# Kernel tuning notes

Measured on AMD Instinct MI355X. Metric: run time of the kernel, lower is better.

## Reference

```python
import jax, jax.numpy as jnp
import numpy as np

B, C_IN, C_HID, H, W = 4, 512, 512, 64, 64


def setup_inputs() -> dict:
    key = jax.random.key(0)
    ks = jax.random.split(key, 9)
    s_in = 1.0 / np.sqrt(C_IN)
    s_hid = 1.0 / np.sqrt(C_HID)
    return {
        "inp": jax.random.normal(ks[0], (B, C_IN, H, W), dtype=jnp.float32),
        "Wk": jax.random.normal(ks[1], (C_HID, C_IN), dtype=jnp.float32) * s_in,
        "bk": jax.random.normal(ks[2], (C_HID,), dtype=jnp.float32) * 0.01,
        "Wq": jax.random.normal(ks[3], (C_HID, C_IN), dtype=jnp.float32) * s_in,
        "bq": jax.random.normal(ks[4], (C_HID,), dtype=jnp.float32) * 0.01,
        "Wv": jax.random.normal(ks[5], (C_HID, C_IN), dtype=jnp.float32) * s_in,
        "bv": jax.random.normal(ks[6], (C_HID,), dtype=jnp.float32) * 0.01,
        "Wo": jax.random.normal(ks[7], (C_IN, C_HID), dtype=jnp.float32) * s_hid,
        "bo": jax.random.normal(ks[8], (C_IN,), dtype=jnp.float32) * 0.01,
    }


def reference(inp, Wk, bk, Wq, bq, Wv, bv, Wo, bo):
    b, _, h, w = inp.shape
    n = h * w

    def conv1x1(x, Wt, bias):  # 1x1 conv == per-pixel GEMM
        return jnp.einsum('bchw,oc->bohw', x, Wt) + bias[None, :, None, None]

    k = conv1x1(inp, Wk, bk).reshape(b, C_HID, n)   # [B,Ch,N]
    q = conv1x1(inp, Wq, bq).reshape(b, C_HID, n)
    v = conv1x1(inp, Wv, bv).reshape(b, C_HID, n)

    scale = 1.0 / jnp.sqrt(jnp.asarray(C_HID, dtype=jnp.float32))
    # weight[b,i,j] = <key_i, query_j> / sqrt(Ch); softmax over j (dim=2)
    scores = jnp.einsum('bci,bcj->bij', k, q) * scale  # [B,N,N]
    weight = jax.nn.softmax(scores, axis=2)
    # out[b,c,i] = sum_j weight[b,i,j] * v[b,c,j]
    out = jnp.einsum('bij,bcj->bci', weight, v).reshape(b, C_HID, h, w)
    return conv1x1(out, Wo, bo)  # [B,C_in,H,W]
```

## Files before the change

kernel.cpp:

```cpp
#include <hip/hip_runtime.h>
#include <hip/hip_bf16.h>


typedef __attribute__((ext_vector_type(4))) float f32x4;
typedef __attribute__((ext_vector_type(8))) short short8;
typedef __attribute__((ext_vector_type(4))) short short4v;

#define QSCALE 0.06376639774f

__device__ __forceinline__ unsigned short f2bf(float f) {
  unsigned u = __builtin_bit_cast(unsigned, f);
  unsigned r = (u + 0x7FFFu + ((u >> 16) & 1u)) >> 16;
  return (unsigned short)r;
}

__device__ __forceinline__ void gll16(const void* g, void* l) {
  __builtin_amdgcn_global_load_lds((const __attribute__((address_space(1))) void*)g,
                                   (__attribute__((address_space(3))) void*)l, 16, 0, 0);
}

__device__ __forceinline__ void gemm_core(const short* __restrict__ A, int lda,
                                          const short* __restrict__ B, int ldb,
                                          int nk, short* lds, f32x4 (&acc)[4][4]) {
  const int tid = threadIdx.x, w = tid >> 6, lane = tid & 63;
  const int g = lane >> 4, l15 = lane & 15;
  const int wr = w >> 1, wc = w & 1;
  const int rsub = lane >> 2, slot = lane & 3;
  char* la = (char*)lds;
  char* lb = (char*)(lds + 128 * 32);
  for (int ki = 0; ki < nk; ++ki) {
    const int k0 = ki * 32;
    __syncthreads();
#pragma unroll
    for (int q = 0; q < 2; ++q) {
      int qq = w * 2 + q;
      int row = qq * 16 + rsub;
      int soff = ((slot ^ (row & 3)) * 16);
      gll16((const char*)(A + (size_t)row * lda + k0) + soff, la + qq * 1024);
      gll16((const char*)(B + (size_t)row * ldb + k0) + soff, lb + qq * 1024);
    }
    __syncthreads();
    short8 am[4], bn[4];
#pragma unroll
    for (int m = 0; m < 4; ++m) {
      int row = wr * 64 + m * 16 + l15;
      am[m] = *(const short8*)(la + row * 64 + ((g * 16) ^ ((l15 & 3) << 4)));
    }
#pragma unroll
    for (int n = 0; n < 4; ++n) {
      int row = wc * 64 + n * 16 + l15;
      bn[n] = *(const short8*)(lb + row * 64 + ((g * 16) ^ ((l15 & 3) << 4)));
    }
#pragma unroll
    for (int m = 0; m < 4; ++m)
#pragma unroll
      for (int n = 0; n < 4; ++n)
        acc[m][n] = __builtin_amdgcn_mfma_f32_16x16x32_bf16(am[m], bn[n], acc[m][n], 0, 0, 0);
  }
}

#define BOUNCE_WRITE(lds2, row, col, val) \
  (lds2)[(row) * 128 + ((col) ^ (((row) & 7) << 3))] = (val)

#define BOUNCE_FLUSH(lds2, gbase, pitch)                                        \
  do {                                                                          \
    __syncthreads();                                                            \
    _Pragma("unroll")                                                           \
    for (int it_ = 0; it_ < 8; ++it_) {                                         \
      int row_ = (threadIdx.x >> 4) + it_ * 16;                                 \
      short8 v_ = *(const short8*)&(lds2)[row_ * 128 +                          \
                      (((threadIdx.x & 15) * 8) ^ ((row_ & 7) << 3))];          \
      *(short8*)((gbase) + (size_t)row_ * (pitch) + (threadIdx.x & 15) * 8) = v_;\
    }                                                                           \
  } while (0)

__global__ __launch_bounds__(256) void cvt_w_kernel(
    const float* __restrict__ wk, const float* __restrict__ wq,
    const float* __restrict__ wv, const float* __restrict__ wo,
    short* __restrict__ o) {
  int z = blockIdx.y;
  const float* s = (z == 0) ? wk : (z == 1) ? wq : (z == 2) ? wv : wo;
  int i = blockIdx.x * 256 + threadIdx.x;
  float4 f = ((const float4*)s)[i];
  short4v v;
  v[0] = (short)f2bf(f.x); v[1] = (short)f2bf(f.y);
  v[2] = (short)f2bf(f.z); v[3] = (short)f2bf(f.w);
  if (z < 3) {
    *(short4v*)(o + z * 262144 + i * 4) = v;
  } else {
    int idx = i * 4, co = idx >> 9, cc = idx & 511;
    short* base = o + 786432 + co * 1024 + cc;
    *(short4v*)base = v;
    *(short4v*)(base + 512) = v;
  }
}

__global__ __launch_bounds__(256) void transpose_x_kernel(
    const float* __restrict__ inp, short* __restrict__ xt) {
  __shared__ float t[32][33];
  int tx = threadIdx.x, ty = threadIdx.y;
  int n0 = blockIdx.x * 32, c0 = blockIdx.y * 32, b = blockIdx.z;
  const float* src = inp + ((size_t)(b * 512 + c0)) * 4096 + n0;
#pragma unroll
  for (int r = 0; r < 4; ++r) t[ty + r * 8][tx] = src[(ty + r * 8) * 4096 + tx];
  __syncthreads();
  short* dst = xt + ((size_t)((b << 12) + n0)) * 512 + c0;
#pragma unroll
  for (int r = 0; r < 4; ++r) dst[(ty + r * 8) * 512 + tx] = (short)f2bf(t[tx][ty + r * 8]);
}

__global__ __launch_bounds__(256) void gemm_kqv_kernel(
    const short* __restrict__ xt,
    const short* __restrict__ wk, const short* __restrict__ wq, const short* __restrict__ wv,
    const float* __restrict__ bk, const float* __restrict__ bq, const float* __restrict__ bv,
    short* __restrict__ kt, short* __restrict__ qt, short* __restrict__ vc) {
  const int z = blockIdx.z;
  __shared__ short lds[2 * 128 * 32];
  __shared__ short lds2[128 * 128];
  const short *A, *B;
  int arow0, brow0;
  if (z < 2) { arow0 = blockIdx.x * 128; brow0 = blockIdx.y * 128;
               A = xt + (size_t)arow0 * 512; B = ((z == 0) ? wk : wq) + (size_t)brow0 * 512; }
  else       { arow0 = blockIdx.y * 128; brow0 = blockIdx.x * 128;
               A = wv + (size_t)arow0 * 512; B = xt + (size_t)brow0 * 512; }
  f32x4 acc[4][4] = {};
  gemm_core(A, 512, B, 512, 16, lds, acc);
  const int tid = threadIdx.x, w = tid >> 6, lane = tid & 63;
  const int g = lane >> 4, l15 = lane & 15;
  const int wr = w >> 1, wc = w & 1;
#pragma unroll
  for (int m = 0; m < 4; ++m)
#pragma unroll
    for (int n = 0; n < 4; ++n)
#pragma unroll
      for (int r = 0; r < 4; ++r) {
        int row = wr * 64 + m * 16 + g * 4 + r, col = wc * 64 + n * 16 + l15;
        float v = acc[m][n][r], val;
        if (z == 0)      val = (v + bk[brow0 + col]) * QSCALE;
        else if (z == 1) val = v + bq[brow0 + col];
        else             val = v + bv[arow0 + row];
        BOUNCE_WRITE(lds2, row, col, (short)f2bf(val));
      }
  short* gbase; int pitch;
  if (z == 0)      { gbase = kt + (size_t)arow0 * 512 + brow0; pitch = 512; }
  else if (z == 1) { gbase = qt + (size_t)arow0 * 512 + brow0; pitch = 512; }
  else             { gbase = vc + (size_t)arow0 * 16384 + brow0; pitch = 16384; }
  BOUNCE_FLUSH(lds2, gbase, pitch);
}

__global__ __launch_bounds__(256) void gemm_s_kernel(
    const short* __restrict__ kt, const short* __restrict__ qt,
    short* __restrict__ P, float* __restrict__ Lpart) {
  __shared__ short lds[2 * 128 * 32];
  __shared__ short lds2[128 * 128];
  const int b = blockIdx.z & 3, h = blockIdx.z >> 2;
  const int i0 = blockIdx.y * 128, jl0 = blockIdx.x * 128;
  const int jg0 = h * 2048 + jl0;
  const short* A = kt + ((size_t)(b << 12) + i0) * 512;
  const short* B = qt + ((size_t)(b << 12) + jg0) * 512;
  f32x4 acc[4][4] = {};
  gemm_core(A, 512, B, 512, 16, lds, acc);
  const int tid = threadIdx.x, w = tid >> 6, lane = tid & 63;
  const int g = lane >> 4, l15 = lane & 15;
  const int wr = w >> 1, wc = w & 1;
  float rs[4][4];
#pragma unroll
  for (int m = 0; m < 4; ++m)
#pragma unroll
    for (int r = 0; r < 4; ++r) rs[m][r] = 0.f;
#pragma unroll
  for (int m = 0; m < 4; ++m)
#pragma unroll
    for (int n = 0; n < 4; ++n)
#pragma unroll
      for (int r = 0; r < 4; ++r) {
        float p = exp2f(acc[m][n][r]);
        rs[m][r] += p;
        int row = wr * 64 + m * 16 + g * 4 + r, col = wc * 64 + n * 16 + l15;
        BOUNCE_WRITE(lds2, row, col, (short)f2bf(p));
      }
  const int jp = (jg0 >> 6) + wc;
  float* Lp = Lpart + (((size_t)b * 64 + jp) << 12) + i0 + wr * 64;
#pragma unroll
  for (int m = 0; m < 4; ++m)
#pragma unroll
    for (int r = 0; r < 4; ++r) {
      float s = rs[m][r];
      s += __shfl_xor(s, 1); s += __shfl_xor(s, 2);
      s += __shfl_xor(s, 4); s += __shfl_xor(s, 8);
      if (l15 == 0) Lp[m * 16 + g * 4 + r] = s;
    }
  short* gbase = P + (size_t)h * 33554432 + ((size_t)((b << 12) + i0)) * 2048 + jl0;
  BOUNCE_FLUSH(lds2, gbase, 2048);
}

__global__ __launch_bounds__(256) void gemm_pv_kernel(
    const short* __restrict__ P, const short* __restrict__ vc,
    short* __restrict__ otab) {
  __shared__ short lds[2 * 128 * 32];
  __shared__ short lds2[128 * 128];
  const int bid = blockIdx.x;
  const int xcd = bid & 7, s = bid >> 3;
  const int c = s & 3, gi = (s >> 2) * 8 + xcd;
  const int i = gi & 31, bh = gi >> 5;
  const int b = bh & 3, h = bh >> 2;
  const int i0 = i * 128, c0 = c * 128;
  const short* A = P + (size_t)h * 33554432 + ((size_t)((b << 12) + i0)) * 2048;
  const short* B = vc + (size_t)c0 * 16384 + (b << 12) + h * 2048;
  f32x4 acc[4][4] = {};
  gemm_core(A, 2048, B, 16384, 64, lds, acc);
  const int tid = threadIdx.x, w = tid >> 6, lane = tid & 63;
  const int g = lane >> 4, l15 = lane & 15;
  const int wr = w >> 1, wc = w & 1;
#pragma unroll
  for (int m = 0; m < 4; ++m)
#pragma unroll
    for (int n = 0; n < 4; ++n)
#pragma unroll
      for (int r = 0; r < 4; ++r) {
        int row = wr * 64 + m * 16 + g * 4 + r, col = wc * 64 + n * 16 + l15;
        BOUNCE_WRITE(lds2, row, col, (short)f2bf(acc[m][n][r]));
      }
  short* gbase = otab + ((size_t)((b << 12) + i0)) * 1024 + h * 512 + c0;
  BOUNCE_FLUSH(lds2, gbase, 1024);
}

__global__ __launch_bounds__(256) void lred_kernel(
    const float* __restrict__ Lpart, float* __restrict__ linv) {
  int i = blockIdx.x * 256 + threadIdx.x;
  int b = i >> 12;
  float s = 0.f;
#pragma unroll 8
  for (int jp = 0; jp < 64; ++jp) s += Lpart[(((size_t)b * 64 + jp) << 12) + (i & 4095)];
  linv[i] = 1.0f / s;
}

__global__ __launch_bounds__(256) void gemm_out_kernel(
    const short* __restrict__ wdup, const short* __restrict__ otab,
    const float* __restrict__ bo, const float* __restrict__ linv,
    float* __restrict__ out) {
  __shared__ short lds[2 * 128 * 32];
  const int b = blockIdx.z;
  const int arow0 = blockIdx.y * 128;
  const int bn0 = blockIdx.x * 128;
  const short* A = wdup + (size_t)arow0 * 1024;
  const short* B = otab + ((size_t)((b << 12) + bn0)) * 1024;
  f32x4 acc[4][4] = {};
  gemm_core(A, 1024, B, 1024, 32, lds, acc);
  const int tid = threadIdx.x, w = tid >> 6, lane = tid & 63;
  const int g = lane >> 4, l15 = lane & 15;
  const int wr = w >> 1, wc = w & 1;
#pragma unroll
  for (int m = 0; m < 4; ++m) {
    int co = arow0 + wr * 64 + m * 16 + g * 4;
#pragma unroll
    for (int n = 0; n < 4; ++n) {
      int nl = bn0 + wc * 64 + n * 16 + l15;
      float li = linv[(b << 12) + nl];
#pragma unroll
      for (int r = 0; r < 4; ++r)
        out[((size_t)(b * 512 + co + r) << 12) + nl] = acc[m][n][r] * li + bo[co + r];
    }
  }
}

extern "C" void kernel_launch(void* const* d_in, const int* in_sizes, int n_in,
                              void* d_out, int out_size, void* d_ws, size_t ws_size,
                              hipStream_t stream) {
  const float* inp = (const float*)d_in[0];
  const float* Wk = (const float*)d_in[1];
  const float* bk = (const float*)d_in[2];
  const float* Wq = (const float*)d_in[3];
  const float* bq = (const float*)d_in[4];
  const float* Wv = (const float*)d_in[5];
  const float* bv = (const float*)d_in[6];
  const float* Wo = (const float*)d_in[7];
  const float* bo = (const float*)d_in[8];
  float* out = (float*)d_out;
  char* ws = (char*)d_ws;
  const size_t MB = 1048576;
  short* kt    = (short*)(ws);
  short* qt    = (short*)(ws + 16 * MB);
  short* vc    = (short*)(ws + 32 * MB);
  short* wb    = (short*)(ws + 48 * MB);
  short* xt    = (short*)(ws + 51 * MB);
  float* Lpart = (float*)(ws + 51 * MB);
  float* linv  = (float*)(ws + 55 * MB);
  short* P     = (short*)(ws + 67 * MB);
  short* otab  = (short*)(ws + 195 * MB);

  (void)in_sizes; (void)n_in; (void)out_size; (void)ws_size;

  cvt_w_kernel<<<dim3(256, 4), 256, 0, stream>>>(Wk, Wq, Wv, Wo, wb);
  transpose_x_kernel<<<dim3(128, 16, 4), dim3(32, 8, 1), 0, stream>>>(inp, xt);
  gemm_kqv_kernel<<<dim3(128, 4, 3), 256, 0, stream>>>(
      xt, wb, wb + 262144, wb + 524288, bk, bq, bv, kt, qt, vc);
  gemm_s_kernel<<<dim3(16, 32, 8), 256, 0, stream>>>(kt, qt, P, Lpart);
  gemm_pv_kernel<<<dim3(1024), 256, 0, stream>>>(P, vc, otab);
  lred_kernel<<<64, 256, 0, stream>>>(Lpart, linv);
  gemm_out_kernel<<<dim3(32, 4, 4), 256, 0, stream>>>(wb + 786432, otab, bo, linv, out);
}
```

Before: 317.7 us.

## Use 256x256 double-buffered 8-wave GEMM tiles for score and PV kernels

Adds a new 256x256-tile GEMM core with 512 threads, a 64-wide K step, double-buffered LDS staging through global_load_lds, explicit vmcnt waits and s_setprio around MFMA groups. The score (exp) kernel and the PV kernel switch to this core with 128KB of dynamic LDS, which cuts global traffic per FLOP and overlaps the loads for the next tiles with compute. The KQV kernel now aliases its bounce buffer onto the staging LDS to reduce shared-memory use. The cost is a much larger LDS footprint and fewer blocks in the PV grid (256 blocks), which may leave CUs idle.

```diff
diff --git a/kernel.cpp b/kernel.cpp
--- a/kernel.cpp
+++ b/kernel.cpp
@@ -7,6 +7,8 @@
 typedef __attribute__((ext_vector_type(4))) short short4v;
 
 #define QSCALE 0.06376639774f
+#define FENCE asm volatile("" ::: "memory")
+#define SBAR  __builtin_amdgcn_s_barrier()
 
 __device__ __forceinline__ unsigned short f2bf(float f) {
   unsigned u = __builtin_bit_cast(unsigned, f);
@@ -17,6 +19,113 @@
 __device__ __forceinline__ void gll16(const void* g, void* l) {
   __builtin_amdgcn_global_load_lds((const __attribute__((address_space(1))) void*)g,
                                    (__attribute__((address_space(3))) void*)l, 16, 0, 0);
+}
+
+#define MFMA_BF16(d, va, vb) \
+  d = __builtin_amdgcn_mfma_f32_16x16x32_bf16(va, vb, d, 0, 0, 0)
+
+__device__ __forceinline__ void gemm256_core(
+    const short* __restrict__ A, int lda,
+    const short* __restrict__ B, int ldb,
+    int nkt, char* sm, f32x4 (&acc)[8][4]) {
+  const int tid = threadIdx.x, w = tid >> 6, lane = tid & 63;
+  const int g = lane >> 4, l15 = lane & 15;
+  const int wm = w >> 2, wn = w & 3;
+  const int swz = (l15 & 7) << 4;
+  const int brow = (wn & 1) << 6;
+
+  auto stageA = [&](int buf, int h, int kt) {
+    char* dst = sm + (((buf << 1) | h) << 14) + (w << 10);
+    const char* gs = (const char*)A + ((size_t)(h * 128) * lda + (size_t)kt * 64) * 2;
+#pragma unroll
+    for (int q = 0; q < 2; ++q) {
+      int o = (q << 13) | (w << 10) | (lane << 4);
+      int row = o >> 7, cb = (o & 127) ^ ((row & 7) << 4);
+      gll16(gs + (size_t)row * (lda * 2) + cb, dst + (q << 13));
+    }
+  };
+  auto stageB = [&](int buf, int h, int kt) {
+    char* dst = sm + 65536 + (((buf << 1) | h) << 14) + (w << 10);
+    const char* gs = (const char*)B + ((size_t)(h * 128) * ldb + (size_t)kt * 64) * 2;
+#pragma unroll
+    for (int q = 0; q < 2; ++q) {
+      int o = (q << 13) | (w << 10) | (lane << 4);
+      int row = o >> 7, cb = (o & 127) ^ ((row & 7) << 4);
+      gll16(gs + (size_t)row * (ldb * 2) + cb, dst + (q << 13));
+    }
+  };
+
+  stageA(0, 0, 0); stageA(0, 1, 0); stageB(0, 0, 0); stageB(0, 1, 0);
+  stageA(1, 0, 1); stageA(1, 1, 1); stageB(1, 0, 1); stageB(1, 1, 1);
+  asm volatile("s_waitcnt vmcnt(8)" ::: "memory");
+  SBAR; FENCE;
+
+  for (int t = 0; t < nkt; ++t) {
+    const int buf = t & 1;
+    const char* SA = sm + (((buf << 1) | wm) << 14);
+    const char* SB = sm + 65536 + (((buf << 1) | (wn >> 1)) << 14);
+    short8 a[8][2], b[4][2];
+#pragma unroll
+    for (int mf = 0; mf < 8; ++mf)
+      a[mf][0] = *(const short8*)(SA + (mf * 16 + l15) * 128 + ((g * 16) ^ swz));
+#pragma unroll
+    for (int nf = 0; nf < 4; ++nf)
+      b[nf][0] = *(const short8*)(SB + (brow + nf * 16 + l15) * 128 + ((g * 16) ^ swz));
+#pragma unroll
+    for (int mf = 0; mf < 8; ++mf)
+      a[mf][1] = *(const short8*)(SA + (mf * 16 + l15) * 128 + ((64 + g * 16) ^ swz));
+#pragma unroll
+    for (int nf = 0; nf < 4; ++nf)
+      b[nf][1] = *(const short8*)(SB + (brow + nf * 16 + l15) * 128 + ((64 + g * 16) ^ swz));
+    __builtin_amdgcn_s_setprio(1);
+#pragma unroll
+    for (int mf = 0; mf < 4; ++mf)
+#pragma unroll
+      for (int nf = 0; nf < 4; ++nf)
+        MFMA_BF16(acc[mf][nf], a[mf][0], b[nf][0]);
+    __builtin_amdgcn_s_setprio(0);
+    asm volatile("s_waitcnt lgkmcnt(0)" ::: "memory");
+    SBAR; FENCE;
+    if (t + 2 < nkt) { stageA(buf, 0, t + 2); stageA(buf, 1, t + 2); }
+    __builtin_amdgcn_s_setprio(1);
+#pragma unroll
+    for (int mf = 4; mf < 8; ++mf)
+#pragma unroll
+      for (int nf = 0; nf < 4; ++nf)
+        MFMA_BF16(acc[mf][nf], a[mf][0], b[nf][0]);
+    __builtin_amdgcn_s_setprio(0);
+    if (t + 2 < nkt) { stageB(buf, 0, t + 2); stageB(buf, 1, t + 2); }
+    __builtin_amdgcn_s_setprio(1);
+#pragma unroll
+    for (int mf = 0; mf < 4; ++mf)
+#pragma unroll
+      for (int nf = 0; nf < 4; ++nf)
+        MFMA_BF16(acc[mf][nf], a[mf][1], b[nf][1]);
+#pragma unroll
+    for (int mf = 4; mf < 8; ++mf)
+#pragma unroll
+      for (int nf = 0; nf < 4; ++nf)
+        MFMA_BF16(acc[mf][nf], a[mf][1], b[nf][1]);
+    __builtin_amdgcn_s_setprio(0);
+    if (t + 2 < nkt)      asm volatile("s_waitcnt vmcnt(8)" ::: "memory");
+    else if (t + 1 < nkt) asm volatile("s_waitcnt vmcnt(0)" ::: "memory");
+    SBAR; FENCE;
+  }
+}
+
+#define BOUNCE256_WRITE(smp, row, colb, val) \
+  *(short*)((smp) + (row) * 512 + (((colb)) ^ (((row) & 7) << 4))) = (val)
+
+__device__ __forceinline__ void bounce256_flush(const char* smp, short* gbase,
+                                                int pitch ) {
+  const int tid = threadIdx.x;
+  SBAR; FENCE;
+#pragma unroll
+  for (int it = 0; it < 16; ++it) {
+    int row = (tid >> 5) + it * 16;
+    short8 v = *(const short8*)(smp + row * 512 + (((tid & 31) * 16) ^ ((row & 7) << 4)));
+    *(short8*)(gbase + (size_t)row * pitch + (tid & 31) * 8) = v;
+  }
 }
 
 __device__ __forceinline__ void gemm_core(const short* __restrict__ A, int lda,
@@ -55,7 +164,7 @@
     for (int m = 0; m < 4; ++m)
 #pragma unroll
       for (int n = 0; n < 4; ++n)
-        acc[m][n] = __builtin_amdgcn_mfma_f32_16x16x32_bf16(am[m], bn[n], acc[m][n], 0, 0, 0);
+        MFMA_BF16(acc[m][n], am[m], bn[n]);
   }
 }
 
@@ -115,8 +224,9 @@
     const float* __restrict__ bk, const float* __restrict__ bq, const float* __restrict__ bv,
     short* __restrict__ kt, short* __restrict__ qt, short* __restrict__ vc) {
   const int z = blockIdx.z;
-  __shared__ short lds[2 * 128 * 32];
-  __shared__ short lds2[128 * 128];
+  __shared__ char smk[32768];
+  short* lds = (short*)smk;
+  short* lds2 = (short*)smk;
   const short *A, *B;
   int arow0, brow0;
   if (z < 2) { arow0 = blockIdx.x * 128; brow0 = blockIdx.y * 128;
@@ -128,6 +238,7 @@
   const int tid = threadIdx.x, w = tid >> 6, lane = tid & 63;
   const int g = lane >> 4, l15 = lane & 15;
   const int wr = w >> 1, wc = w & 1;
+  __syncthreads();
 #pragma unroll
   for (int m = 0; m < 4; ++m)
 #pragma unroll
@@ -148,81 +259,71 @@
   BOUNCE_FLUSH(lds2, gbase, pitch);
 }
 
-__global__ __launch_bounds__(256) void gemm_s_kernel(
+__global__ __launch_bounds__(512, 2) void gemm_s256_kernel(
     const short* __restrict__ kt, const short* __restrict__ qt,
     short* __restrict__ P, float* __restrict__ Lpart) {
-  __shared__ short lds[2 * 128 * 32];
-  __shared__ short lds2[128 * 128];
+  extern __shared__ char sm[];
   const int b = blockIdx.z & 3, h = blockIdx.z >> 2;
-  const int i0 = blockIdx.y * 128, jl0 = blockIdx.x * 128;
-  const int jg0 = h * 2048 + jl0;
+  const int i0 = blockIdx.y * 256, jt0 = blockIdx.x * 256;
   const short* A = kt + ((size_t)(b << 12) + i0) * 512;
-  const short* B = qt + ((size_t)(b << 12) + jg0) * 512;
-  f32x4 acc[4][4] = {};
-  gemm_core(A, 512, B, 512, 16, lds, acc);
-  const int tid = threadIdx.x, w = tid >> 6, lane = tid & 63;
-  const int g = lane >> 4, l15 = lane & 15;
-  const int wr = w >> 1, wc = w & 1;
-  float rs[4][4];
-#pragma unroll
-  for (int m = 0; m < 4; ++m)
-#pragma unroll
-    for (int r = 0; r < 4; ++r) rs[m][r] = 0.f;
-#pragma unroll
-  for (int m = 0; m < 4; ++m)
-#pragma unroll
-    for (int n = 0; n < 4; ++n)
+  const short* B = qt + ((size_t)((b << 12) + h * 2048 + jt0)) * 512;
+  f32x4 acc[8][4] = {};
+  gemm256_core(A, 512, B, 512, 8, sm, acc);
+  const int tid = threadIdx.x, w = tid >> 6, lane = tid & 63;
+  const int g = lane >> 4, l15 = lane & 15;
+  const int wm = w >> 2, wn = w & 3;
+  const int jp = (h * 2048 + jt0 + wn * 64) >> 6;
+  float* Lp = Lpart + (((size_t)b * 64 + jp) << 12) + i0 + wm * 128;
+#pragma unroll
+  for (int mf = 0; mf < 8; ++mf) {
+    float psum[4] = {0.f, 0.f, 0.f, 0.f};
+#pragma unroll
+    for (int nf = 0; nf < 4; ++nf)
 #pragma unroll
       for (int r = 0; r < 4; ++r) {
-        float p = exp2f(acc[m][n][r]);
-        rs[m][r] += p;
-        int row = wr * 64 + m * 16 + g * 4 + r, col = wc * 64 + n * 16 + l15;
-        BOUNCE_WRITE(lds2, row, col, (short)f2bf(p));
+        float p = exp2f(acc[mf][nf][r]);
+        psum[r] += p;
+        int row = wm * 128 + mf * 16 + g * 4 + r;
+        int colb = (wn * 64 + nf * 16 + l15) * 2;
+        BOUNCE256_WRITE(sm, row, colb, (short)f2bf(p));
       }
-  const int jp = (jg0 >> 6) + wc;
-  float* Lp = Lpart + (((size_t)b * 64 + jp) << 12) + i0 + wr * 64;
-#pragma unroll
-  for (int m = 0; m < 4; ++m)
 #pragma unroll
     for (int r = 0; r < 4; ++r) {
-      float s = rs[m][r];
+      float s = psum[r];
       s += __shfl_xor(s, 1); s += __shfl_xor(s, 2);
       s += __shfl_xor(s, 4); s += __shfl_xor(s, 8);
-      if (l15 == 0) Lp[m * 16 + g * 4 + r] = s;
-    }
-  short* gbase = P + (size_t)h * 33554432 + ((size_t)((b << 12) + i0)) * 2048 + jl0;
-  BOUNCE_FLUSH(lds2, gbase, 2048);
-}
-
-__global__ __launch_bounds__(256) void gemm_pv_kernel(
+      if (l15 == 0) Lp[mf * 16 + g * 4 + r] = s;
+    }
+  }
+  short* gbase = P + (size_t)h * 33554432 + ((size_t)((b << 12) + i0)) * 2048 + jt0;
+  bounce256_flush(sm, gbase, 2048);
+}
+
+__global__ __launch_bounds__(512, 2) void gemm_pv256_kernel(
     const short* __restrict__ P, const short* __restrict__ vc,
     short* __restrict__ otab) {
-  __shared__ short lds[2 * 128 * 32];
-  __shared__ short lds2[128 * 128];
-  const int bid = blockIdx.x;
-  const int xcd = bid & 7, s = bid >> 3;
-  const int c = s & 3, gi = (s >> 2) * 8 + xcd;
-  const int i = gi & 31, bh = gi >> 5;
-  const int b = bh & 3, h = bh >> 2;
-  const int i0 = i * 128, c0 = c * 128;
+  extern __shared__ char sm[];
+  const int b = blockIdx.z & 3, h = blockIdx.z >> 2;
+  const int i0 = blockIdx.y * 256, c0 = blockIdx.x * 256;
   const short* A = P + (size_t)h * 33554432 + ((size_t)((b << 12) + i0)) * 2048;
   const short* B = vc + (size_t)c0 * 16384 + (b << 12) + h * 2048;
-  f32x4 acc[4][4] = {};
-  gemm_core(A, 2048, B, 16384, 64, lds, acc);
-  const int tid = threadIdx.x, w = tid >> 6, lane = tid & 63;
-  const int g = lane >> 4, l15 = lane & 15;
-  const int wr = w >> 1, wc = w & 1;
-#pragma unroll
-  for (int m = 0; m < 4; ++m)
-#pragma unroll
-    for (int n = 0; n < 4; ++n)
+  f32x4 acc[8][4] = {};
+  gemm256_core(A, 2048, B, 16384, 32, sm, acc);
+  const int tid = threadIdx.x, w = tid >> 6, lane = tid & 63;
+  const int g = lane >> 4, l15 = lane & 15;
+  const int wm = w >> 2, wn = w & 3;
+#pragma unroll
+  for (int mf = 0; mf < 8; ++mf)
+#pragma unroll
+    for (int nf = 0; nf < 4; ++nf)
 #pragma unroll
       for (int r = 0; r < 4; ++r) {
-        int row = wr * 64 + m * 16 + g * 4 + r, col = wc * 64 + n * 16 + l15;
-        BOUNCE_WRITE(lds2, row, col, (short)f2bf(acc[m][n][r]));
+        int row = wm * 128 + mf * 16 + g * 4 + r;
+        int colb = (wn * 64 + nf * 16 + l15) * 2;
+        BOUNCE256_WRITE(sm, row, colb, (short)f2bf(acc[mf][nf][r]));
       }
   short* gbase = otab + ((size_t)((b << 12) + i0)) * 1024 + h * 512 + c0;
-  BOUNCE_FLUSH(lds2, gbase, 1024);
+  bounce256_flush(sm, gbase, 1024);
 }
 
 __global__ __launch_bounds__(256) void lred_kernel(
@@ -291,12 +392,17 @@
 
   (void)in_sizes; (void)n_in; (void)out_size; (void)ws_size;
 
+  hipFuncSetAttribute((const void*)gemm_s256_kernel,
+                      hipFuncAttributeMaxDynamicSharedMemorySize, 131072);
+  hipFuncSetAttribute((const void*)gemm_pv256_kernel,
+                      hipFuncAttributeMaxDynamicSharedMemorySize, 131072);
+
   cvt_w_kernel<<<dim3(256, 4), 256, 0, stream>>>(Wk, Wq, Wv, Wo, wb);
   transpose_x_kernel<<<dim3(128, 16, 4), dim3(32, 8, 1), 0, stream>>>(inp, xt);
   gemm_kqv_kernel<<<dim3(128, 4, 3), 256, 0, stream>>>(
       xt, wb, wb + 262144, wb + 524288, bk, bq, bv, kt, qt, vc);
-  gemm_s_kernel<<<dim3(16, 32, 8), 256, 0, stream>>>(kt, qt, P, Lpart);
-  gemm_pv_kernel<<<dim3(1024), 256, 0, stream>>>(P, vc, otab);
+  gemm_s256_kernel<<<dim3(8, 16, 8), 512, 131072, stream>>>(kt, qt, P, Lpart);
+  gemm_pv256_kernel<<<dim3(2, 16, 8), 512, 131072, stream>>>(P, vc, otab);
   lred_kernel<<<64, 256, 0, stream>>>(Lpart, linv);
   gemm_out_kernel<<<dim3(32, 4, 4), 256, 0, stream>>>(wb + 786432, otab, bo, linv, out);
 }
```

After: 274.8 us. 13.5% less time.

## Drop LDS bounce epilogues and remap GEMM grids with XCD-aware block ordering

Applied to the files above, without the earlier changes.

Removes the LDS staging buffer used to coalesce bf16 epilogue stores in the KQV, score, PV kernels and writes results directly to global memory per lane. All GEMM launches become 1D grids whose block index is decoded so blocks sharing a batch/half or panel land on the same XCD, aiming at better L2 locality. Direct scalar 2-byte stores free LDS and a barrier but produce poorly coalesced writes, notably for the large P matrix.

```diff
diff --git a/kernel.cpp b/kernel.cpp
--- a/kernel.cpp
+++ b/kernel.cpp
@@ -18,6 +18,9 @@
   __builtin_amdgcn_global_load_lds((const __attribute__((address_space(1))) void*)g,
                                    (__attribute__((address_space(3))) void*)l, 16, 0, 0);
 }
+
+#define MFMA_BF16(d, va, vb) \
+  d = __builtin_amdgcn_mfma_f32_16x16x32_bf16(va, vb, d, 0, 0, 0)
 
 __device__ __forceinline__ void gemm_core(const short* __restrict__ A, int lda,
                                           const short* __restrict__ B, int ldb,
@@ -55,24 +58,9 @@
     for (int m = 0; m < 4; ++m)
 #pragma unroll
       for (int n = 0; n < 4; ++n)
-        acc[m][n] = __builtin_amdgcn_mfma_f32_16x16x32_bf16(am[m], bn[n], acc[m][n], 0, 0, 0);
+        MFMA_BF16(acc[m][n], am[m], bn[n]);
   }
 }
-
-#define BOUNCE_WRITE(lds2, row, col, val) \
-  (lds2)[(row) * 128 + ((col) ^ (((row) & 7) << 3))] = (val)
-
-#define BOUNCE_FLUSH(lds2, gbase, pitch)                                        \
-  do {                                                                          \
-    __syncthreads();                                                            \
-    _Pragma("unroll")                                                           \
-    for (int it_ = 0; it_ < 8; ++it_) {                                         \
-      int row_ = (threadIdx.x >> 4) + it_ * 16;                                 \
-      short8 v_ = *(const short8*)&(lds2)[row_ * 128 +                          \
-                      (((threadIdx.x & 15) * 8) ^ ((row_ & 7) << 3))];          \
-      *(short8*)((gbase) + (size_t)row_ * (pitch) + (threadIdx.x & 15) * 8) = v_;\
-    }                                                                           \
-  } while (0)
 
 __global__ __launch_bounds__(256) void cvt_w_kernel(
     const float* __restrict__ wk, const float* __restrict__ wq,
@@ -109,20 +97,29 @@
   for (int r = 0; r < 4; ++r) dst[(ty + r * 8) * 512 + tx] = (short)f2bf(t[tx][ty + r * 8]);
 }
 
-__global__ __launch_bounds__(256) void gemm_kqv_kernel(
+__global__ __launch_bounds__(256) void kqv_kernel(
     const short* __restrict__ xt,
     const short* __restrict__ wk, const short* __restrict__ wq, const short* __restrict__ wv,
     const float* __restrict__ bk, const float* __restrict__ bq, const float* __restrict__ bv,
     short* __restrict__ kt, short* __restrict__ qt, short* __restrict__ vc) {
-  const int z = blockIdx.z;
   __shared__ short lds[2 * 128 * 32];
-  __shared__ short lds2[128 * 128];
+  const int bid = blockIdx.x;
+  const int xcd = bid & 7, s = bid >> 3;
+  const int pg = s / 12, t = s % 12;
+  const int panel = pg * 8 + xcd;
+  const int z = t >> 2;
+  const int ct = t & 3;
   const short *A, *B;
   int arow0, brow0;
-  if (z < 2) { arow0 = blockIdx.x * 128; brow0 = blockIdx.y * 128;
-               A = xt + (size_t)arow0 * 512; B = ((z == 0) ? wk : wq) + (size_t)brow0 * 512; }
-  else       { arow0 = blockIdx.y * 128; brow0 = blockIdx.x * 128;
-               A = wv + (size_t)arow0 * 512; B = xt + (size_t)brow0 * 512; }
+  if (z < 2) {
+    arow0 = panel * 128; brow0 = ct * 128;
+    A = xt + (size_t)arow0 * 512;
+    B = ((z == 0) ? wk : wq) + (size_t)brow0 * 512;
+  } else {
+    arow0 = ct * 128; brow0 = panel * 128;
+    A = wv + (size_t)arow0 * 512;
+    B = xt + (size_t)brow0 * 512;
+  }
   f32x4 acc[4][4] = {};
   gemm_core(A, 512, B, 512, 16, lds, acc);
   const int tid = threadIdx.x, w = tid >> 6, lane = tid & 63;
@@ -134,40 +131,40 @@
     for (int n = 0; n < 4; ++n)
 #pragma unroll
       for (int r = 0; r < 4; ++r) {
-        int row = wr * 64 + m * 16 + g * 4 + r, col = wc * 64 + n * 16 + l15;
-        float v = acc[m][n][r], val;
-        if (z == 0)      val = (v + bk[brow0 + col]) * QSCALE;
-        else if (z == 1) val = v + bq[brow0 + col];
-        else             val = v + bv[arow0 + row];
-        BOUNCE_WRITE(lds2, row, col, (short)f2bf(val));
+        int row = wr * 64 + m * 16 + g * 4 + r;
+        int col = wc * 64 + n * 16 + l15;
+        float v = acc[m][n][r];
+        if (z == 0)      kt[(size_t)(arow0 + row) * 512 + brow0 + col] =
+                           (short)f2bf((v + bk[brow0 + col]) * QSCALE);
+        else if (z == 1) qt[(size_t)(arow0 + row) * 512 + brow0 + col] =
+                           (short)f2bf(v + bq[brow0 + col]);
+        else             vc[(size_t)(arow0 + row) * 16384 + brow0 + col] =
+                           (short)f2bf(v + bv[arow0 + row]);
       }
-  short* gbase; int pitch;
-  if (z == 0)      { gbase = kt + (size_t)arow0 * 512 + brow0; pitch = 512; }
-  else if (z == 1) { gbase = qt + (size_t)arow0 * 512 + brow0; pitch = 512; }
-  else             { gbase = vc + (size_t)arow0 * 16384 + brow0; pitch = 16384; }
-  BOUNCE_FLUSH(lds2, gbase, pitch);
 }
 
 __global__ __launch_bounds__(256) void gemm_s_kernel(
     const short* __restrict__ kt, const short* __restrict__ qt,
     short* __restrict__ P, float* __restrict__ Lpart) {
   __shared__ short lds[2 * 128 * 32];
-  __shared__ short lds2[128 * 128];
-  const int b = blockIdx.z & 3, h = blockIdx.z >> 2;
-  const int i0 = blockIdx.y * 128, jl0 = blockIdx.x * 128;
-  const int jg0 = h * 2048 + jl0;
-  const short* A = kt + ((size_t)(b << 12) + i0) * 512;
-  const short* B = qt + ((size_t)(b << 12) + jg0) * 512;
+  const int bid = blockIdx.x;
+  const int xcd = bid & 7, s = bid >> 3;
+  const int b = xcd >> 1, h = xcd & 1;
+  const int it = s >> 4, jt = s & 15;
+  const int i0 = it * 128, jl0 = jt * 128;
+  const short* A = kt + ((size_t)((b << 12) + i0)) * 512;
+  const short* B = qt + ((size_t)((b << 12) + h * 2048 + jl0)) * 512;
   f32x4 acc[4][4] = {};
   gemm_core(A, 512, B, 512, 16, lds, acc);
   const int tid = threadIdx.x, w = tid >> 6, lane = tid & 63;
   const int g = lane >> 4, l15 = lane & 15;
   const int wr = w >> 1, wc = w & 1;
-  float rs[4][4];
-#pragma unroll
-  for (int m = 0; m < 4; ++m)
-#pragma unroll
-    for (int r = 0; r < 4; ++r) rs[m][r] = 0.f;
+  short* Pb = P + (size_t)h * 33554432 + ((size_t)((b << 12) + i0)) * 2048 + jl0;
+  float psum[4][4];
+#pragma unroll
+  for (int m = 0; m < 4; ++m)
+#pragma unroll
+    for (int r = 0; r < 4; ++r) psum[m][r] = 0.f;
 #pragma unroll
   for (int m = 0; m < 4; ++m)
 #pragma unroll
@@ -175,36 +172,33 @@
 #pragma unroll
       for (int r = 0; r < 4; ++r) {
         float p = exp2f(acc[m][n][r]);
-        rs[m][r] += p;
-        int row = wr * 64 + m * 16 + g * 4 + r, col = wc * 64 + n * 16 + l15;
-        BOUNCE_WRITE(lds2, row, col, (short)f2bf(p));
+        psum[m][r] += p;
+        int row = wr * 64 + m * 16 + g * 4 + r;
+        int col = wc * 64 + n * 16 + l15;
+        Pb[(size_t)row * 2048 + col] = (short)f2bf(p);
       }
-  const int jp = (jg0 >> 6) + wc;
+  const int jp = (h * 2048 + jl0 + wc * 64) >> 6;
   float* Lp = Lpart + (((size_t)b * 64 + jp) << 12) + i0 + wr * 64;
 #pragma unroll
   for (int m = 0; m < 4; ++m)
 #pragma unroll
     for (int r = 0; r < 4; ++r) {
-      float s = rs[m][r];
-      s += __shfl_xor(s, 1); s += __shfl_xor(s, 2);
-      s += __shfl_xor(s, 4); s += __shfl_xor(s, 8);
-      if (l15 == 0) Lp[m * 16 + g * 4 + r] = s;
-    }
-  short* gbase = P + (size_t)h * 33554432 + ((size_t)((b << 12) + i0)) * 2048 + jl0;
-  BOUNCE_FLUSH(lds2, gbase, 2048);
+      float ss = psum[m][r];
+      ss += __shfl_xor(ss, 1); ss += __shfl_xor(ss, 2);
+      ss += __shfl_xor(ss, 4); ss += __shfl_xor(ss, 8);
+      if (l15 == 0) Lp[m * 16 + g * 4 + r] = ss;
+    }
 }
 
 __global__ __launch_bounds__(256) void gemm_pv_kernel(
     const short* __restrict__ P, const short* __restrict__ vc,
     short* __restrict__ otab) {
   __shared__ short lds[2 * 128 * 32];
-  __shared__ short lds2[128 * 128];
   const int bid = blockIdx.x;
   const int xcd = bid & 7, s = bid >> 3;
-  const int c = s & 3, gi = (s >> 2) * 8 + xcd;
-  const int i = gi & 31, bh = gi >> 5;
-  const int b = bh & 3, h = bh >> 2;
-  const int i0 = i * 128, c0 = c * 128;
+  const int b = xcd >> 1, h = xcd & 1;
+  const int it = s >> 2, ct = s & 3;
+  const int i0 = it * 128, c0 = ct * 128;
   const short* A = P + (size_t)h * 33554432 + ((size_t)((b << 12) + i0)) * 2048;
   const short* B = vc + (size_t)c0 * 16384 + (b << 12) + h * 2048;
   f32x4 acc[4][4] = {};
@@ -212,17 +206,17 @@
   const int tid = threadIdx.x, w = tid >> 6, lane = tid & 63;
   const int g = lane >> 4, l15 = lane & 15;
   const int wr = w >> 1, wc = w & 1;
+  short* Ob = otab + ((size_t)((b << 12) + i0)) * 1024 + h * 512 + c0;
 #pragma unroll
   for (int m = 0; m < 4; ++m)
 #pragma unroll
     for (int n = 0; n < 4; ++n)
 #pragma unroll
       for (int r = 0; r < 4; ++r) {
-        int row = wr * 64 + m * 16 + g * 4 + r, col = wc * 64 + n * 16 + l15;
-        BOUNCE_WRITE(lds2, row, col, (short)f2bf(acc[m][n][r]));
+        int row = wr * 64 + m * 16 + g * 4 + r;
+        int col = wc * 64 + n * 16 + l15;
+        Ob[(size_t)row * 1024 + col] = (short)f2bf(acc[m][n][r]);
       }
-  short* gbase = otab + ((size_t)((b << 12) + i0)) * 1024 + h * 512 + c0;
-  BOUNCE_FLUSH(lds2, gbase, 1024);
 }
 
 __global__ __launch_bounds__(256) void lred_kernel(
@@ -240,9 +234,13 @@
     const float* __restrict__ bo, const float* __restrict__ linv,
     float* __restrict__ out) {
   __shared__ short lds[2 * 128 * 32];
-  const int b = blockIdx.z;
-  const int arow0 = blockIdx.y * 128;
-  const int bn0 = blockIdx.x * 128;
+  const int bid = blockIdx.x;
+  const int xcd = bid & 7, s = bid >> 3;
+  const int b = xcd >> 1, ch = xcd & 1;
+  const int cot = ch * 2 + (s & 1);
+  const int nt = s >> 1;
+  const int arow0 = cot * 128;
+  const int bn0 = nt * 128;
   const short* A = wdup + (size_t)arow0 * 1024;
   const short* B = otab + ((size_t)((b << 12) + bn0)) * 1024;
   f32x4 acc[4][4] = {};
@@ -293,10 +291,10 @@
 
   cvt_w_kernel<<<dim3(256, 4), 256, 0, stream>>>(Wk, Wq, Wv, Wo, wb);
   transpose_x_kernel<<<dim3(128, 16, 4), dim3(32, 8, 1), 0, stream>>>(inp, xt);
-  gemm_kqv_kernel<<<dim3(128, 4, 3), 256, 0, stream>>>(
+  kqv_kernel<<<1536, 256, 0, stream>>>(
       xt, wb, wb + 262144, wb + 524288, bk, bq, bv, kt, qt, vc);
-  gemm_s_kernel<<<dim3(16, 32, 8), 256, 0, stream>>>(kt, qt, P, Lpart);
-  gemm_pv_kernel<<<dim3(1024), 256, 0, stream>>>(P, vc, otab);
+  gemm_s_kernel<<<4096, 256, 0, stream>>>(kt, qt, P, Lpart);
+  gemm_pv_kernel<<<1024, 256, 0, stream>>>(P, vc, otab);
   lred_kernel<<<64, 256, 0, stream>>>(Lpart, linv);
-  gemm_out_kernel<<<dim3(32, 4, 4), 256, 0, stream>>>(wb + 786432, otab, bo, linv, out);
-}
+  gemm_out_kernel<<<512, 256, 0, stream>>>(wb + 786432, otab, bo, linv, out);
+}
```

New measurement: 299.7 us. -5.7%, faster.
